# Kernel optimization log

Hardware: AMD Instinct MI355X
Metric: run time of the kernel (lower is better)

## Reference

```python
import jax, jax.numpy as jnp
import numpy as np

HID = 64
IN_DIM = 6


def setup_inputs() -> dict:
    key = jax.random.key(0)
    ks = jax.random.split(key, 16)
    B, S, N, D = 8, 32, 64, IN_DIM
    g = lambda k, shape, fan_in: jax.random.normal(k, shape, jnp.float32) / np.sqrt(fan_in)
    return {
        "x": jax.random.normal(ks[0], (B, S, N, D), jnp.float32),
        "emb_w": g(ks[1], (D, HID), D),
        "emb_b": jnp.zeros((HID,), jnp.float32),
        "edge_w1": g(ks[2], (2 * HID + 1, HID), 2 * HID + 1),
        "edge_b1": jnp.zeros((HID,), jnp.float32),
        "edge_w2": g(ks[3], (HID, HID), HID),
        "edge_b2": jnp.zeros((HID,), jnp.float32),
        "node_w1": g(ks[4], (2 * HID, HID), 2 * HID),
        "node_b1": jnp.zeros((HID,), jnp.float32),
        "node_w2": g(ks[5], (HID, HID), HID),
        "node_b2": jnp.zeros((HID,), jnp.float32),
        "coord_w1": g(ks[6], (HID, HID), HID),
        "coord_b1": jnp.zeros((HID,), jnp.float32),
        "coord_w2": g(ks[7], (HID, 1), HID),
        "final_w": g(ks[8], (HID, IN_DIM), HID),
        "final_b": jnp.zeros((IN_DIM,), jnp.float32),
    }


def reference(x, emb_w, emb_b, edge_w1, edge_b1, edge_w2, edge_b2,
              node_w1, node_b1, node_w2, node_b2,
              coord_w1, coord_b1, coord_w2, final_w, final_b):
    B, S, N, D = x.shape
    xf = x.reshape(B * S, N, D)           # [G,N,6]
    pos, vel = xf[..., :3], xf[..., 3:]
    h = xf @ emb_w + emb_b                # [G,N,H]

    rel = pos[:, :, None, :] - pos[:, None, :, :]          # [G,N,N,3]
    dist_sq = jnp.sum(rel * rel, axis=-1, keepdims=True)   # [G,N,N,1]

    H = h.shape[-1]
    h_i = jnp.broadcast_to(h[:, :, None, :], (B * S, N, N, H))
    h_j = jnp.broadcast_to(h[:, None, :, :], (B * S, N, N, H))
    e_in = jnp.concatenate([h_i, h_j, dist_sq], axis=-1)   # [G,N,N,2H+1]
    m_ij = jax.nn.relu(e_in @ edge_w1 + edge_b1) @ edge_w2 + edge_b2  # [G,N,N,H]
    m_i = m_ij.sum(axis=2)                                  # [G,N,H]

    w = jax.nn.relu(m_ij @ coord_w1 + coord_b1) @ coord_w2  # [G,N,N,1]
    pos_out = pos + (rel * w).sum(axis=2) / N

    n_in = jnp.concatenate([h, m_i], axis=-1)
    h = h + jax.nn.relu(n_in @ node_w1 + node_b1) @ node_w2 + node_b2
    vel_out = vel + (h @ final_w + final_b)[..., 3:]

    out = jnp.concatenate([pos_out, vel_out], axis=-1)
    return out.reshape(B, S, N, D)
```

## Files before the change

kernel.cpp:

```cpp
#include <hip/hip_runtime.h>


#define NG 256

typedef __attribute__((ext_vector_type(4))) float f32x4;
typedef __attribute__((ext_vector_type(8))) __bf16 bf16x8;

__device__ __forceinline__ f32x4 mfma16(bf16x8 a, bf16x8 b, f32x4 c){
  return __builtin_amdgcn_mfma_f32_16x16x32_bf16(a, b, c, 0, 0, 0);
}

__device__ __forceinline__ void fma4x4(float* acc, float4 a, float4 b){
  acc[0]  += a.x*b.x; acc[1]  += a.x*b.y; acc[2]  += a.x*b.z; acc[3]  += a.x*b.w;
  acc[4]  += a.y*b.x; acc[5]  += a.y*b.y; acc[6]  += a.y*b.z; acc[7]  += a.y*b.w;
  acc[8]  += a.z*b.x; acc[9]  += a.z*b.y; acc[10] += a.z*b.z; acc[11] += a.z*b.w;
  acc[12] += a.w*b.x; acc[13] += a.w*b.y; acc[14] += a.w*b.z; acc[15] += a.w*b.w;
}

__global__ __launch_bounds__(512)
void egnn_edge_mfma(const float* __restrict__ x,
    const float* __restrict__ emb_w,  const float* __restrict__ emb_b,
    const float* __restrict__ edge_w1,const float* __restrict__ edge_b1,
    const float* __restrict__ edge_w2,const float* __restrict__ edge_b2,
    const float* __restrict__ coord_w1,const float* __restrict__ coord_b1,
    const float* __restrict__ coord_w2,
    float* __restrict__ out, float* __restrict__ ws_mi)
{
  __shared__ __align__(16) float  sAB [64*64];
  __shared__ __align__(16) __bf16 sC  [64*72];
  __shared__ __align__(16) __bf16 sW3t[64*72];
  __shared__ __align__(16) __bf16 sW2t[64*72];
  __shared__ __align__(16) __bf16 sTr [64*72];
  __shared__ float sDsq[8][64];
  __shared__ float sPX[64], sPY[64], sPZ[64];
  __shared__ __align__(16) float sW1L[64];
  __shared__ float sCB1p[64], sCW2[64], sB2[64], sB1[64];
  __shared__ __align__(16) float sW1a[64*64], sW1b[64*64], sW2T[64*64], sCW1[64*64];
  __shared__ __align__(16) float sHt[64*64];
  __shared__ float sXL[384], sEW[384], sEB[64];

  const int bs  = blockIdx.x, tid = threadIdx.x;
  const int lane = tid & 63, wv = tid >> 6;
  const float* xg = x + bs*384;

  if (tid < 384){ sXL[tid] = xg[tid]; sEW[tid] = emb_w[tid]; }
  if (tid < 64){
    sEB[tid] = emb_b[tid];  sB1[tid] = edge_b1[tid]; sB2[tid] = edge_b2[tid];
    sCW2[tid] = coord_w2[tid]; sW1L[tid] = edge_w1[128*64 + tid];
  } else if (tid < 128){
    int j = tid-64; sPX[j]=xg[j*6]; sPY[j]=xg[j*6+1]; sPZ[j]=xg[j*6+2];
  }
  {
    const float4* w1 = (const float4*)edge_w1;
    const float4* cw = (const float4*)coord_w1;
    float4* da=(float4*)sW1a; float4* db=(float4*)sW1b; float4* dc=(float4*)sCW1;
    #pragma unroll
    for (int e=0;e<2;e++){ int q=tid+e*512; da[q]=w1[q]; db[q]=w1[1024+q]; dc[q]=cw[q]; }
  }
  #pragma unroll
  for (int e=0;e<8;e++){ int idx=tid+e*512; int n=idx>>6, k=idx&63;
    sW2T[idx] = edge_w2[k*64+n]; }
  __syncthreads();

  #pragma unroll
  for (int e=0;e<8;e++){
    int idx=tid+e*512; int m=idx>>6, j=idx&63;
    float v = sEB[m];
    #pragma unroll
    for (int d=0; d<6; d++) v += sXL[j*6+d]*sEW[d*64+m];
    sHt[idx] = v;
  }
  __syncthreads();

  const int g = tid>>8, tl = tid&255, tjx = tl>>4, tnx = tl&15;
  {
    float acc[16] = {};
    const float* Bm = g ? sW1b : sW1a;
    #pragma unroll 8
    for (int k=0;k<64;k++){
      float4 av = *(const float4*)&sHt[k*64 + 4*tjx];
      float4 bv = *(const float4*)&Bm [k*64 + 4*tnx];
      fma4x4(acc, av, bv);
    }
    if (g==0){
      #pragma unroll
      for (int r=0;r<4;r++)
        #pragma unroll
        for (int c=0;c<4;c++)
          sAB[(4*tjx+r)*64 + 4*tnx+c] = acc[r*4+c] + sB1[4*tnx+c];
    } else {
      #pragma unroll
      for (int r=0;r<4;r++)
        #pragma unroll
        for (int c=0;c<4;c++)
          sC[(4*tjx+r)*72 + 4*tnx+c] = (__bf16)acc[r*4+c];
    }
  }
  if (g==0){
    float acc[16] = {};
    #pragma unroll 8
    for (int k=0;k<64;k++){
      float4 av = *(const float4*)&sW2T[k*64 + 4*tjx];
      float4 bv = *(const float4*)&sCW1[k*64 + 4*tnx];
      fma4x4(acc, av, bv);
    }
    #pragma unroll
    for (int r=0;r<4;r++)
      #pragma unroll
      for (int c=0;c<4;c++)
        sW3t[(4*tnx+c)*72 + 4*tjx+r] = (__bf16)acc[r*4+c];
  } else {
    #pragma unroll
    for (int e=0;e<16;e++){ int idx=tl+e*256; sW2t[(idx>>6)*72 + (idx&63)] = (__bf16)sW2T[idx]; }
    if (tl < 64){
      float s = coord_b1[tl];
      for (int n=0;n<64;n++) s += sB2[n]*sCW1[n*64+tl];
      sCB1p[tl] = s;
    }
  }
  __syncthreads();

  const int lg = lane>>4, ln = lane&15;

  for (int ib=0; ib<8; ib++){
    const int i = ib*8 + wv;
    {
      float dx=sPX[i]-sPX[lane], dy=sPY[i]-sPY[lane], dz=sPZ[i]-sPZ[lane];
      sDsq[wv][lane] = dx*dx+dy*dy+dz*dz;
    }
    float ab8[2][8];
    #pragma unroll
    for (int kb=0;kb<2;kb++){
      *(float4*)&ab8[kb][0] = *(const float4*)&sAB[i*64 + kb*32+lg*8];
      *(float4*)&ab8[kb][4] = *(const float4*)&sAB[i*64 + kb*32+lg*8+4];
    }
    float trs[2][8];
    #pragma unroll
    for (int kb=0;kb<2;kb++)
      #pragma unroll
      for (int e=0;e<8;e++) trs[kb][e]=0.f;

    float sw=0.f, swx=0.f, swy=0.f, swz=0.f;

    #pragma unroll
    for (int jt=0;jt<4;jt++){
      const int j = jt*16 + ln;
      const float dq = sDsq[wv][j];
      f32x4 a4[4];
      #pragma unroll
      for (int nt=0;nt<4;nt++) a4[nt] = f32x4{0.f,0.f,0.f,0.f};

      #pragma unroll
      for (int kb=0;kb<2;kb++){
        bf16x8 c8 = *(const bf16x8*)&sC[j*72 + kb*32 + lg*8];
        float w8[8];
        *(float4*)&w8[0] = *(const float4*)&sW1L[kb*32+lg*8];
        *(float4*)&w8[4] = *(const float4*)&sW1L[kb*32+lg*8+4];
        bf16x8 t8;
        #pragma unroll
        for (int e=0;e<8;e++){
          float v = ab8[kb][e] + (float)c8[e] + dq*w8[e];
          v = fmaxf(v, 0.f);
          trs[kb][e] += v;
          t8[e] = (__bf16)v;
        }
        #pragma unroll
        for (int nt=0;nt<4;nt++){
          bf16x8 b8 = *(const bf16x8*)&sW3t[(nt*16+ln)*72 + kb*32 + lg*8];
          a4[nt] = mfma16(t8, b8, a4[nt]);
        }
      }

      float wr[4];
      #pragma unroll
      for (int r=0;r<4;r++){
        float p = 0.f;
        #pragma unroll
        for (int nt=0;nt<4;nt++){
          int n = nt*16 + ln;
          float u = a4[nt][r] + sCB1p[n];
          p += fmaxf(u, 0.f)*sCW2[n];
        }
        p += __shfl_xor(p,1); p += __shfl_xor(p,2);
        p += __shfl_xor(p,4); p += __shfl_xor(p,8);
        wr[r] = p;
      }
      #pragma unroll
      for (int r=0;r<4;r++){
        int jj = jt*16 + lg*4 + r;
        sw  += wr[r];
        swx += wr[r]*sPX[jj];
        swy += wr[r]*sPY[jj];
        swz += wr[r]*sPZ[jj];
      }
    }

    #pragma unroll
    for (int kb=0;kb<2;kb++)
      #pragma unroll
      for (int e=0;e<8;e++){
        float s = trs[kb][e];
        s += __shfl_xor(s,1); s += __shfl_xor(s,2);
        s += __shfl_xor(s,4); s += __shfl_xor(s,8);
        trs[kb][e] = s;
      }
    if (ln == 0){
      #pragma unroll
      for (int kb=0;kb<2;kb++){
        bf16x8 t8;
        #pragma unroll
        for (int e=0;e<8;e++) t8[e] = (__bf16)trs[kb][e];
        *(bf16x8*)&sTr[i*72 + kb*32 + lg*8] = t8;
      }
    }

    sw  += __shfl_xor(sw,16);  sw  += __shfl_xor(sw,32);
    swx += __shfl_xor(swx,16); swx += __shfl_xor(swx,32);
    swy += __shfl_xor(swy,16); swy += __shfl_xor(swy,32);
    swz += __shfl_xor(swz,16); swz += __shfl_xor(swz,32);
    if (lane == 0){
      float* o = out + (bs*64 + i)*6;
      o[0] = sPX[i] + (sPX[i]*sw - swx)*(1.f/64.f);
      o[1] = sPY[i] + (sPY[i]*sw - swy)*(1.f/64.f);
      o[2] = sPZ[i] + (sPZ[i]*sw - swz)*(1.f/64.f);
    }
  }

  __syncthreads();
  #pragma unroll
  for (int t2=0;t2<2;t2++){
    int t  = wv*2 + t2;
    int it = t>>2, nt = t&3;
    f32x4 a2 = f32x4{0.f,0.f,0.f,0.f};
    #pragma unroll
    for (int kb=0;kb<2;kb++){
      bf16x8 a8 = *(const bf16x8*)&sTr [(it*16+ln)*72 + kb*32 + lg*8];
      bf16x8 b8 = *(const bf16x8*)&sW2t[(nt*16+ln)*72 + kb*32 + lg*8];
      a2 = mfma16(a8, b8, a2);
    }
    int n = nt*16 + ln;
    float b2n = 64.f*sB2[n];
    #pragma unroll
    for (int r=0;r<4;r++){
      int i = it*16 + lg*4 + r;
      ws_mi[(bs*64 + i)*64 + n] = a2[r] + b2n;
    }
  }
}

__global__ __launch_bounds__(256)
void egnn_node_mfma(const float* __restrict__ x,
    const float* __restrict__ emb_w,  const float* __restrict__ emb_b,
    const float* __restrict__ node_w1,const float* __restrict__ node_b1,
    const float* __restrict__ node_w2,const float* __restrict__ node_b2,
    const float* __restrict__ final_w,const float* __restrict__ final_b,
    float* __restrict__ out, const float* __restrict__ ws_mi)
{
  __shared__ __align__(16) float  sHt [64*64];
  __shared__ __align__(16) __bf16 sAb [64*136];
  __shared__ __align__(16) __bf16 sNW1t[64*136];
  __shared__ __align__(16) float sNW2[64*64];
  __shared__ float sG  [64*4];
  __shared__ float sHf3[64*4];
  __shared__ float sFW3[64*4];
  __shared__ float sCvec[4];
  __shared__ float sXL[384], sEW[384], sEB[64], sNB1[64], sNB2[64];

  const int bs=blockIdx.x, tid=threadIdx.x;
  const int lane=tid&63, wv=tid>>6, ln=lane&15, lg=lane>>4;
  const float* xg = x + bs*384;

  for (int q=tid;q<384;q+=256){ sXL[q]=xg[q]; sEW[q]=emb_w[q]; }
  if (tid<64){ sEB[tid]=emb_b[tid]; sNB1[tid]=node_b1[tid]; sNB2[tid]=node_b2[tid]; }
  if (tid<192){ int n=tid&63, d=tid>>6; sFW3[n*4+d]=final_w[n*6+3+d]; }
  { const float4* g2=(const float4*)node_w2; float4* d2=(float4*)sNW2;
    #pragma unroll
    for (int e=0;e<4;e++) d2[tid+e*256]=g2[tid+e*256]; }
  #pragma unroll
  for (int e=0;e<32;e++){ int idx=tid+e*256; int kk=idx>>6, n=idx&63;
    sNW1t[n*136+kk]=(__bf16)node_w1[idx]; }
  { const float* mig = ws_mi + bs*4096;
    #pragma unroll
    for (int e=0;e<16;e++){ int idx=tid+e*256; int i=idx>>6, n=idx&63;
      sAb[i*136+64+n]=(__bf16)mig[idx]; } }
  __syncthreads();

  { int j=tid&63, mb=tid>>6;
    #pragma unroll
    for (int mm=0;mm<16;mm++){ int m=mb*16+mm;
      float v=sEB[m];
      #pragma unroll
      for (int d=0;d<6;d++) v+=sXL[j*6+d]*sEW[d*64+m];
      sHt[m*64+j]=v; sAb[j*136+m]=(__bf16)v; } }
  __syncthreads();

  if (tid<192){
    int k=tid&63, d=tid>>6;
    float gacc=0.f, s=0.f;
    for (int nn=0;nn<64;nn++){
      int n=(nn+k)&63;
      gacc += sNW2[k*64+n]*sFW3[n*4+d];
      s    += sHt[nn*64+k]*sFW3[nn*4+d];
    }
    sG[k*4+d]=gacc; sHf3[k*4+d]=s;
  } else if (tid<195){
    int d=tid-192; float c=final_b[3+d];
    for (int n=0;n<64;n++) c+=sNB2[n]*sFW3[n*4+d];
    sCvec[d]=c;
  }
  __syncthreads();

  f32x4 acc[4];
  #pragma unroll
  for (int nt=0;nt<4;nt++) acc[nt]=f32x4{0.f,0.f,0.f,0.f};
  #pragma unroll
  for (int kb=0;kb<4;kb++){
    bf16x8 a8 = *(const bf16x8*)&sAb[(wv*16+ln)*136 + kb*32 + lg*8];
    #pragma unroll
    for (int nt=0;nt<4;nt++){
      bf16x8 b8 = *(const bf16x8*)&sNW1t[(nt*16+ln)*136 + kb*32 + lg*8];
      acc[nt]=mfma16(a8,b8,acc[nt]);
    }
  }
  float p[4][3];
  #pragma unroll
  for(int r=0;r<4;r++){ p[r][0]=0.f; p[r][1]=0.f; p[r][2]=0.f; }
  #pragma unroll
  for (int nt=0;nt<4;nt++){
    int n=nt*16+ln;
    float zb=sNB1[n];
    float g0=sG[n*4], g1=sG[n*4+1], g2=sG[n*4+2];
    #pragma unroll
    for (int r=0;r<4;r++){
      float u=fmaxf(acc[nt][r]+zb,0.f);
      p[r][0]+=u*g0; p[r][1]+=u*g1; p[r][2]+=u*g2;
    }
  }
  #pragma unroll
  for (int off=1;off<16;off<<=1)
    #pragma unroll
    for (int r=0;r<4;r++){
      p[r][0]+=__shfl_xor(p[r][0],off);
      p[r][1]+=__shfl_xor(p[r][1],off);
      p[r][2]+=__shfl_xor(p[r][2],off);
    }
  if (ln==0){
    #pragma unroll
    for (int r=0;r<4;r++){
      int j=wv*16+lg*4+r; int base=(bs*64+j)*6;
      #pragma unroll
      for (int d=0;d<3;d++)
        out[base+3+d]=xg[j*6+3+d]+sHf3[j*4+d]+sCvec[d]+p[r][d];
    }
  }
}

extern "C" void kernel_launch(void* const* d_in, const int* in_sizes, int n_in,
                              void* d_out, int out_size, void* d_ws, size_t ws_size,
                              hipStream_t stream)
{
  const float* x        = (const float*)d_in[0];
  const float* emb_w    = (const float*)d_in[1];
  const float* emb_b    = (const float*)d_in[2];
  const float* edge_w1  = (const float*)d_in[3];
  const float* edge_b1  = (const float*)d_in[4];
  const float* edge_w2  = (const float*)d_in[5];
  const float* edge_b2  = (const float*)d_in[6];
  const float* node_w1  = (const float*)d_in[7];
  const float* node_b1  = (const float*)d_in[8];
  const float* node_w2  = (const float*)d_in[9];
  const float* node_b2  = (const float*)d_in[10];
  const float* coord_w1 = (const float*)d_in[11];
  const float* coord_b1 = (const float*)d_in[12];
  const float* coord_w2 = (const float*)d_in[13];
  const float* final_w  = (const float*)d_in[14];
  const float* final_b  = (const float*)d_in[15];
  float* out   = (float*)d_out;
  float* ws_mi = (float*)d_ws;

  egnn_edge_mfma<<<NG, 512, 0, stream>>>(x, emb_w, emb_b,
      edge_w1, edge_b1, edge_w2, edge_b2, coord_w1, coord_b1, coord_w2,
      out, ws_mi);
  egnn_node_mfma<<<NG, 256, 0, stream>>>(x, emb_w, emb_b,
      node_w1, node_b1, node_w2, node_b2, final_w, final_b,
      out, ws_mi);
}
```

Measured before the change: 70.60 us.

## Stream weights from global memory and alias shared buffers to cut LDS footprint

Drops the shared-memory staging of edge_w1, coord_w1 and the transposed edge_w2. The small GEMMs now read these weights directly from global memory (L1/L2 cached), and sHt, sTr and sDsq share one aliased buffer, so LDS use per block falls from roughly 130KB to about 50KB. The intent is to let more blocks reside per CU and to remove a staging phase and a barrier. The trade-off is uncoalesced or repeated global reads in the prologue, and a W2·CW1 product computed per thread with scalar loops.

```diff
diff --git a/kernel.cpp b/kernel.cpp
--- a/kernel.cpp
+++ b/kernel.cpp
@@ -30,14 +30,15 @@
   __shared__ __align__(16) __bf16 sC  [64*72];
   __shared__ __align__(16) __bf16 sW3t[64*72];
   __shared__ __align__(16) __bf16 sW2t[64*72];
-  __shared__ __align__(16) __bf16 sTr [64*72];
-  __shared__ float sDsq[8][64];
+  __shared__ __align__(16) unsigned char uniRaw[16384];
   __shared__ float sPX[64], sPY[64], sPZ[64];
   __shared__ __align__(16) float sW1L[64];
   __shared__ float sCB1p[64], sCW2[64], sB2[64], sB1[64];
-  __shared__ __align__(16) float sW1a[64*64], sW1b[64*64], sW2T[64*64], sCW1[64*64];
-  __shared__ __align__(16) float sHt[64*64];
   __shared__ float sXL[384], sEW[384], sEB[64];
+
+  float*  sHt  = (float*)uniRaw;
+  __bf16* sTr  = (__bf16*)uniRaw;
+  float*  sDsq = (float*)(uniRaw + 9216);
 
   const int bs  = blockIdx.x, tid = threadIdx.x;
   const int lane = tid & 63, wv = tid >> 6;
@@ -50,16 +51,6 @@
   } else if (tid < 128){
     int j = tid-64; sPX[j]=xg[j*6]; sPY[j]=xg[j*6+1]; sPZ[j]=xg[j*6+2];
   }
-  {
-    const float4* w1 = (const float4*)edge_w1;
-    const float4* cw = (const float4*)coord_w1;
-    float4* da=(float4*)sW1a; float4* db=(float4*)sW1b; float4* dc=(float4*)sCW1;
-    #pragma unroll
-    for (int e=0;e<2;e++){ int q=tid+e*512; da[q]=w1[q]; db[q]=w1[1024+q]; dc[q]=cw[q]; }
-  }
-  #pragma unroll
-  for (int e=0;e<8;e++){ int idx=tid+e*512; int n=idx>>6, k=idx&63;
-    sW2T[idx] = edge_w2[k*64+n]; }
   __syncthreads();
 
   #pragma unroll
@@ -68,18 +59,39 @@
     float v = sEB[m];
     #pragma unroll
     for (int d=0; d<6; d++) v += sXL[j*6+d]*sEW[d*64+m];
-    sHt[idx] = v;
-  }
-  __syncthreads();
-
-  const int g = tid>>8, tl = tid&255, tjx = tl>>4, tnx = tl&15;
+    sHt[m*64+j] = v;
+  }
   {
+    int k = tid>>3, c0 = (tid&7)*8;
+    float a8[8] = {};
+    for (int n=0;n<64;n++){
+      float w = edge_w2[k*64+n];
+      float4 b0 = *(const float4*)&coord_w1[n*64+c0];
+      float4 b1 = *(const float4*)&coord_w1[n*64+c0+4];
+      a8[0]+=w*b0.x; a8[1]+=w*b0.y; a8[2]+=w*b0.z; a8[3]+=w*b0.w;
+      a8[4]+=w*b1.x; a8[5]+=w*b1.y; a8[6]+=w*b1.z; a8[7]+=w*b1.w;
+    }
+    #pragma unroll
+    for (int cc=0;cc<8;cc++) sW3t[(c0+cc)*72 + k] = (__bf16)a8[cc];
+  }
+  #pragma unroll
+  for (int e=0;e<8;e++){ int idx=tid+e*512; int n=idx>>6, k=idx&63;
+    sW2t[n*72+k] = (__bf16)edge_w2[k*64+n]; }
+  if (tid < 64){
+    float s = coord_b1[tid];
+    for (int n=0;n<64;n++) s += sB2[n]*coord_w1[n*64+tid];
+    sCB1p[tid] = s;
+  }
+  __syncthreads();
+
+  {
+    const int g = tid>>8, tl = tid&255, tjx = tl>>4, tnx = tl&15;
     float acc[16] = {};
-    const float* Bm = g ? sW1b : sW1a;
-    #pragma unroll 8
-    for (int k=0;k<64;k++){
-      float4 av = *(const float4*)&sHt[k*64 + 4*tjx];
-      float4 bv = *(const float4*)&Bm [k*64 + 4*tnx];
+    const float* W = edge_w1 + (g ? 4096 : 0);
+    #pragma unroll 4
+    for (int m=0;m<64;m++){
+      float4 av = *(const float4*)&sHt[m*64 + 4*tjx];
+      float4 bv = *(const float4*)&W  [m*64 + 4*tnx];
       fma4x4(acc, av, bv);
     }
     if (g==0){
@@ -94,28 +106,6 @@
         #pragma unroll
         for (int c=0;c<4;c++)
           sC[(4*tjx+r)*72 + 4*tnx+c] = (__bf16)acc[r*4+c];
-    }
-  }
-  if (g==0){
-    float acc[16] = {};
-    #pragma unroll 8
-    for (int k=0;k<64;k++){
-      float4 av = *(const float4*)&sW2T[k*64 + 4*tjx];
-      float4 bv = *(const float4*)&sCW1[k*64 + 4*tnx];
-      fma4x4(acc, av, bv);
-    }
-    #pragma unroll
-    for (int r=0;r<4;r++)
-      #pragma unroll
-      for (int c=0;c<4;c++)
-        sW3t[(4*tnx+c)*72 + 4*tjx+r] = (__bf16)acc[r*4+c];
-  } else {
-    #pragma unroll
-    for (int e=0;e<16;e++){ int idx=tl+e*256; sW2t[(idx>>6)*72 + (idx&63)] = (__bf16)sW2T[idx]; }
-    if (tl < 64){
-      float s = coord_b1[tl];
-      for (int n=0;n<64;n++) s += sB2[n]*sCW1[n*64+tl];
-      sCB1p[tl] = s;
     }
   }
   __syncthreads();
@@ -126,7 +116,7 @@
     const int i = ib*8 + wv;
     {
       float dx=sPX[i]-sPX[lane], dy=sPY[i]-sPY[lane], dz=sPZ[i]-sPZ[lane];
-      sDsq[wv][lane] = dx*dx+dy*dy+dz*dz;
+      sDsq[wv*64+lane] = dx*dx+dy*dy+dz*dz;
     }
     float ab8[2][8];
     #pragma unroll
@@ -145,7 +135,7 @@
     #pragma unroll
     for (int jt=0;jt<4;jt++){
       const int j = jt*16 + ln;
-      const float dq = sDsq[wv][j];
+      const float dq = sDsq[wv*64+j];
       f32x4 a4[4];
       #pragma unroll
       for (int nt=0;nt<4;nt++) a4[nt] = f32x4{0.f,0.f,0.f,0.f};
```

New measurement: 95.37 us. 35.1% more time.
